# Optimization experiments

Hardware: AMD Instinct MI355X
Metric: run time of the kernel (lower is better)

## Reference

```python
import math
import jax, jax.numpy as jnp
import numpy as np

N_NODES = 50000
N_EDGES = 800000
F_IN = 512
HID = 64
N_CLS = 64
NITER = 10


def setup_inputs() -> dict:
    key = jax.random.key(0)
    k = jax.random.split(key, 6)
    x = jax.random.normal(k[0], (N_NODES, F_IN), jnp.float32)
    edge_index = jax.random.randint(k[1], (2, N_EDGES), 0, N_NODES, jnp.int64)
    W1 = jax.random.normal(k[2], (F_IN, HID), jnp.float32) / np.sqrt(F_IN)
    b1 = jnp.zeros((HID,), jnp.float32)
    W2 = jax.random.normal(k[3], (HID, N_CLS), jnp.float32) / np.sqrt(HID)
    b2 = jnp.zeros((N_CLS,), jnp.float32)
    halt_w = jax.random.normal(k[4], (N_CLS,), jnp.float32) / np.sqrt(N_CLS)
    # reset_parameters: bias = log((1/(niter+1)) / (1 - 1/(niter+1)))
    b = math.log((1.0 / (NITER + 1)) / (1.0 - 1.0 / (NITER + 1)))
    halt_b = jnp.full((1,), b, jnp.float32)
    return {"x": x, "edge_index": edge_index, "W1": W1, "b1": b1,
            "W2": W2, "b2": b2, "halt_w": halt_w, "halt_b": halt_b}


def reference(x, edge_index, W1, b1, W2, b2, halt_w, halt_b):
    N = x.shape[0]
    # MLP (eval mode: dropout is identity)
    h = jnp.maximum(x @ W1 + b1, 0.0)
    local = h @ W2 + b2                      # [N, C] local predictions
    # GCN normalization with self-loops (eval: no edge dropout)
    loops = jnp.arange(N, dtype=edge_index.dtype)
    row = jnp.concatenate([edge_index[0], loops])
    col = jnp.concatenate([edge_index[1], loops])
    deg = jnp.zeros((N,), x.dtype).at[row].add(1.0)
    dis = jnp.where(deg > 0, jax.lax.rsqrt(jnp.maximum(deg, 1.0)), 0.0)
    norm = dis[row] * dis[col]               # [E+N]

    def step(carry, _):
        prop, steps, sum_h, cont, xacc = carry
        old = prop
        msg = norm[:, None] * prop[row]                       # gather + scale
        prop = jax.ops.segment_sum(msg, col, num_segments=N)  # scatter-add
        hh = jax.nn.sigmoid(prop @ halt_w + halt_b[0])        # [N]
        prob = (sum_h + hh < 0.99) & cont
        pf = prob.astype(x.dtype)
        steps = steps + pf
        sum_h = sum_h + pf * hh
        cond = prob & (steps < NITER)
        p = jnp.where(cond, sum_h, 1.0 - sum_h)
        xacc = xacc + (prop * p[:, None] + old * (1.0 - p)[:, None]) * cont.astype(x.dtype)[:, None]
        cont = cont & prob
        return (prop, steps, sum_h, cont, xacc), None

    init = (local, jnp.ones((N,), x.dtype), jnp.zeros((N,), x.dtype),
            jnp.ones((N,), bool), jnp.zeros_like(local))
    (prop, steps, sum_h, cont, xacc), _ = jax.lax.scan(step, init, None, length=NITER)
    out = xacc / steps[:, None]
    return jax.nn.log_softmax(out, axis=1), steps, 1.0 - sum_h
```

## Files before the change

kernel.cpp:

```cpp
#include <hip/hip_runtime.h>
#include <hip/hip_bf16.h>

#define F_IN 512
#define NC 64
#define NITER 10
#define BM 256
#define BK 64

__global__ __launch_bounds__(256) void init_state_kernel(
    float* __restrict__ steps, float* __restrict__ sumh, int* __restrict__ cont,
    int* __restrict__ rowptr, int N, int E) {
  int i = blockIdx.x * blockDim.x + threadIdx.x;
  if (i < N) { steps[i] = 1.0f; sumh[i] = 0.0f; cont[i] = 1; }
  if (i == 0) rowptr[N] = E;
}

__global__ __launch_bounds__(256) void mlp_kernel(
    const float* __restrict__ x, const float* __restrict__ W1,
    const float* __restrict__ b1, const float* __restrict__ W2,
    const float* __restrict__ b2, float* __restrict__ out, int N) {
  __shared__ float xT[BK * BM];
  __shared__ float ws[BK * NC];
  const int tid  = threadIdx.x;
  const int brow = blockIdx.x * BM;
  const int r0 = (tid >> 3) * 8;
  const int c0 = (tid & 7) * 8;

  float acc[8][8];
#pragma unroll
  for (int j = 0; j < 8; ++j) {
    float bv = b1[c0 + j];
#pragma unroll
    for (int i = 0; i < 8; ++i) acc[i][j] = bv;
  }

  for (int kt = 0; kt < F_IN; kt += BK) {
#pragma unroll
    for (int q = 0; q < 16; ++q) {
      int fidx = q * 256 + tid;
      int row = fidx >> 4, kq = fidx & 15;
      int gr = brow + row; if (gr >= N) gr = N - 1;
      float4 v = *reinterpret_cast<const float4*>(&x[(size_t)gr * F_IN + kt + kq * 4]);
      float vv[4] = {v.x, v.y, v.z, v.w};
#pragma unroll
      for (int j = 0; j < 4; ++j) {
        int kk = kq * 4 + j;
        xT[kk * BM + (row ^ (kk & 28))] = vv[j];
      }
    }
#pragma unroll
    for (int q = 0; q < 4; ++q) {
      int fidx = q * 256 + tid;
      int row = fidx >> 4, kq = fidx & 15;
      *reinterpret_cast<float4*>(&ws[row * NC + kq * 4]) =
          *reinterpret_cast<const float4*>(&W1[(size_t)(kt + row) * NC + kq * 4]);
    }
    __syncthreads();
#pragma unroll 4
    for (int k = 0; k < BK; ++k) {
      float4 xa = *reinterpret_cast<const float4*>(&xT[k * BM + (r0 ^ (k & 28))]);
      float4 xb = *reinterpret_cast<const float4*>(&xT[k * BM + ((r0 + 4) ^ (k & 28))]);
      float4 wa = *reinterpret_cast<const float4*>(&ws[k * NC + c0]);
      float4 wb = *reinterpret_cast<const float4*>(&ws[k * NC + c0 + 4]);
      float xr[8] = {xa.x, xa.y, xa.z, xa.w, xb.x, xb.y, xb.z, xb.w};
      float wr[8] = {wa.x, wa.y, wa.z, wa.w, wb.x, wb.y, wb.z, wb.w};
#pragma unroll
      for (int i = 0; i < 8; ++i)
#pragma unroll
        for (int j = 0; j < 8; ++j) acc[i][j] = fmaf(xr[i], wr[j], acc[i][j]);
    }
    __syncthreads();
  }

#pragma unroll
  for (int i = 0; i < 8; ++i)
#pragma unroll
    for (int j = 0; j < 8; ++j) {
      int kk = c0 + j;
      int r  = r0 + i;
      xT[kk * BM + (r ^ (kk & 28))] = fmaxf(acc[i][j], 0.0f);
    }
#pragma unroll
  for (int q = 0; q < 4; ++q) {
    int fidx = q * 256 + tid;
    int row = fidx >> 4, kq = fidx & 15;
    *reinterpret_cast<float4*>(&ws[row * NC + kq * 4]) =
        *reinterpret_cast<const float4*>(&W2[(size_t)row * NC + kq * 4]);
  }
  float acc2[8][8];
#pragma unroll
  for (int j = 0; j < 8; ++j) {
    float bv = b2[c0 + j];
#pragma unroll
    for (int i = 0; i < 8; ++i) acc2[i][j] = bv;
  }
  __syncthreads();
#pragma unroll 4
  for (int k = 0; k < NC; ++k) {
    float4 xa = *reinterpret_cast<const float4*>(&xT[k * BM + (r0 ^ (k & 28))]);
    float4 xb = *reinterpret_cast<const float4*>(&xT[k * BM + ((r0 + 4) ^ (k & 28))]);
    float4 wa = *reinterpret_cast<const float4*>(&ws[k * NC + c0]);
    float4 wb = *reinterpret_cast<const float4*>(&ws[k * NC + c0 + 4]);
    float xr[8] = {xa.x, xa.y, xa.z, xa.w, xb.x, xb.y, xb.z, xb.w};
    float wr[8] = {wa.x, wa.y, wa.z, wa.w, wb.x, wb.y, wb.z, wb.w};
#pragma unroll
    for (int i = 0; i < 8; ++i)
#pragma unroll
      for (int j = 0; j < 8; ++j) acc2[i][j] = fmaf(xr[i], wr[j], acc2[i][j]);
  }
#pragma unroll
  for (int i = 0; i < 8; ++i) {
    int gr = brow + r0 + i;
    if (gr < N) {
      float4 oa = make_float4(acc2[i][0], acc2[i][1], acc2[i][2], acc2[i][3]);
      float4 ob = make_float4(acc2[i][4], acc2[i][5], acc2[i][6], acc2[i][7]);
      *reinterpret_cast<float4*>(&out[(size_t)gr * NC + c0]) = oa;
      *reinterpret_cast<float4*>(&out[(size_t)gr * NC + c0 + 4]) = ob;
    }
  }
}

__global__ __launch_bounds__(256) void hist_kernel(
    const int* __restrict__ ei, int* __restrict__ deg_i,
    int* __restrict__ indeg, int E) {
  int e = blockIdx.x * blockDim.x + threadIdx.x;
  if (e < E) {
    atomicAdd(&deg_i[ei[e]], 1);
    atomicAdd(&indeg[ei[E + e]], 1);
  }
}

__global__ __launch_bounds__(256) void dis_kernel(
    const int* __restrict__ deg_i, float* __restrict__ dis, int N) {
  int i = blockIdx.x * blockDim.x + threadIdx.x;
  if (i < N) dis[i] = 1.0f / sqrtf((float)(deg_i[i] + 1));
}

__global__ __launch_bounds__(256) void scan_sum_kernel(
    const int* __restrict__ indeg, int* __restrict__ bsum, int N) {
  __shared__ int sm[256];
  int tid = threadIdx.x;
  int i = blockIdx.x * 256 + tid;
  sm[tid] = (i < N) ? indeg[i] : 0;
  __syncthreads();
  for (int s = 128; s > 0; s >>= 1) {
    if (tid < s) sm[tid] += sm[tid + s];
    __syncthreads();
  }
  if (tid == 0) bsum[blockIdx.x] = sm[0];
}

__global__ __launch_bounds__(256) void scan_bsum_kernel(int* __restrict__ bsum, int nb) {
  __shared__ int sm[256];
  int tid = threadIdx.x;
  int v = (tid < nb) ? bsum[tid] : 0;
  sm[tid] = v;
  __syncthreads();
  for (int s = 1; s < 256; s <<= 1) {
    int t = (tid >= s) ? sm[tid - s] : 0;
    __syncthreads();
    sm[tid] += t;
    __syncthreads();
  }
  if (tid < nb) bsum[tid] = sm[tid] - v;
}

__global__ __launch_bounds__(256) void scan_final_kernel(
    const int* __restrict__ indeg, const int* __restrict__ bsum,
    int* __restrict__ rowptr, int N) {
  __shared__ int sm[256];
  int tid = threadIdx.x;
  int i = blockIdx.x * 256 + tid;
  int v = (i < N) ? indeg[i] : 0;
  sm[tid] = v;
  __syncthreads();
  for (int s = 1; s < 256; s <<= 1) {
    int t = (tid >= s) ? sm[tid - s] : 0;
    __syncthreads();
    sm[tid] += t;
    __syncthreads();
  }
  if (i < N) rowptr[i] = bsum[blockIdx.x] + sm[tid] - v;
}

__global__ __launch_bounds__(256) void scatter_kernel(
    const int* __restrict__ ei, const int* __restrict__ rowptr,
    int* __restrict__ cursor, const float* __restrict__ dis,
    int2* __restrict__ csr, int E) {
  int e = blockIdx.x * blockDim.x + threadIdx.x;
  if (e < E) {
    int s = ei[e];
    int c = ei[E + e];
    int pos = rowptr[c] + atomicAdd(&cursor[c], 1);
    csr[pos] = make_int2(s, __float_as_int(dis[s] * dis[c]));
  }
}

__global__ __launch_bounds__(256) void prop_step_kernel(
    const float* __restrict__ prop, float* __restrict__ prop_new,
    const int2* __restrict__ csr, const int* __restrict__ rowptr,
    const float* __restrict__ dis, const float* __restrict__ hw,
    const float* __restrict__ hb, float* __restrict__ steps,
    float* __restrict__ sumh, int* __restrict__ cont,
    float* __restrict__ xacc, int N) {
  int wid = (int)((blockIdx.x * blockDim.x + threadIdx.x) >> 6);
  if (wid >= N) return;
  int lane = threadIdx.x & 63;
  size_t rowoff = (size_t)wid * NC + lane;

  float oldv = prop[rowoff];
  float dc = dis[wid];
  int beg = __builtin_amdgcn_readfirstlane(rowptr[wid]);
  int end = __builtin_amdgcn_readfirstlane(rowptr[wid + 1]);

  float a[8];
  a[0] = dc * dc * oldv;
#pragma unroll
  for (int u = 1; u < 8; ++u) a[u] = 0.0f;
  int i = beg;
  for (; i + 8 <= end; i += 8) {
    int2 e[8];
#pragma unroll
    for (int u = 0; u < 8; ++u) e[u] = csr[i + u];
#pragma unroll
    for (int u = 0; u < 8; ++u)
      a[u] = fmaf(__int_as_float(e[u].y), prop[(size_t)e[u].x * NC + lane], a[u]);
  }
  for (; i < end; ++i) {
    int2 e0 = csr[i];
    a[0] = fmaf(__int_as_float(e0.y), prop[(size_t)e0.x * NC + lane], a[0]);
  }
  float acc = ((a[0] + a[1]) + (a[2] + a[3])) + ((a[4] + a[5]) + (a[6] + a[7]));
  prop_new[rowoff] = acc;

  float z = acc * hw[lane];
#pragma unroll
  for (int off = 32; off > 0; off >>= 1) z += __shfl_xor(z, off);
  z += hb[0];
  float hh = 1.0f / (1.0f + expf(-z));

  float st = steps[wid], sh = sumh[wid];
  int ct = cont[wid];
  bool prob = ((sh + hh) < 0.99f) && (ct != 0);
  float pf = prob ? 1.0f : 0.0f;
  st += pf;
  sh += pf * hh;
  bool cond = prob && (st < (float)NITER);
  float pp = cond ? sh : (1.0f - sh);
  float ctf = ct ? 1.0f : 0.0f;
  xacc[rowoff] += (acc * pp + oldv * (1.0f - pp)) * ctf;
  if (lane == 0) { steps[wid] = st; sumh[wid] = sh; cont[wid] = prob ? 1 : 0; }
}

__global__ __launch_bounds__(256) void final_kernel(
    const float* __restrict__ xacc, const float* __restrict__ steps,
    const float* __restrict__ sumh, float* __restrict__ out0,
    float* __restrict__ out1, float* __restrict__ out2, int N) {
  int wid = (int)((blockIdx.x * blockDim.x + threadIdx.x) >> 6);
  if (wid >= N) return;
  int lane = threadIdx.x & 63;
  float st = steps[wid];
  float v = xacc[(size_t)wid * NC + lane] / st;
  float m = v;
#pragma unroll
  for (int off = 32; off > 0; off >>= 1) m = fmaxf(m, __shfl_xor(m, off));
  float e = expf(v - m);
  float s = e;
#pragma unroll
  for (int off = 32; off > 0; off >>= 1) s += __shfl_xor(s, off);
  out0[(size_t)wid * NC + lane] = v - m - logf(s);
  if (lane == 0) { out1[wid] = st; out2[wid] = 1.0f - sumh[wid]; }
}

extern "C" void kernel_launch(void* const* d_in, const int* in_sizes, int n_in,
                              void* d_out, int out_size, void* d_ws, size_t ws_size,
                              hipStream_t stream) {
  const float* x      = (const float*)d_in[0];
  const int*   ei     = (const int*)d_in[1];
  const float* W1     = (const float*)d_in[2];
  const float* b1     = (const float*)d_in[3];
  const float* W2     = (const float*)d_in[4];
  const float* b2     = (const float*)d_in[5];
  const float* halt_w = (const float*)d_in[6];
  const float* halt_b = (const float*)d_in[7];

  const int N = in_sizes[0] / F_IN;
  const int E = in_sizes[1] / 2;

  char* p = (char*)d_ws;
  auto alloc = [&](size_t bytes) {
    void* r = (void*)p;
    p += (bytes + 255) & ~(size_t)255;
    return r;
  };
  float* propA  = (float*)alloc((size_t)N * NC * 4);
  float* propB  = (float*)alloc((size_t)N * NC * 4);
  float* xacc   = (float*)alloc((size_t)N * NC * 4);
  int2*  csr    = (int2*)alloc((size_t)E * 8);
  int*   rowptr = (int*)alloc((size_t)(N + 1) * 4);
  int*   deg_i  = (int*)alloc((size_t)N * 4);
  int*   indeg  = (int*)alloc((size_t)N * 4);
  int*   cursor = (int*)alloc((size_t)N * 4);
  float* dis    = (float*)alloc((size_t)N * 4);
  float* steps  = (float*)alloc((size_t)N * 4);
  float* sumh   = (float*)alloc((size_t)N * 4);
  int*   cont   = (int*)alloc((size_t)N * 4);
  int*   bsum   = (int*)alloc(1024);

  hipMemsetAsync(deg_i,  0, (size_t)N * 4, stream);
  hipMemsetAsync(indeg,  0, (size_t)N * 4, stream);
  hipMemsetAsync(cursor, 0, (size_t)N * 4, stream);
  hipMemsetAsync(xacc,   0, (size_t)N * NC * 4, stream);

  const int nbN = (N + 255) / 256;
  const int nbE = (E + 255) / 256;
  const int nbM = (N + BM - 1) / BM;

  init_state_kernel<<<nbN, 256, 0, stream>>>(steps, sumh, cont, rowptr, N, E);
  mlp_kernel<<<nbM, 256, 0, stream>>>(x, W1, b1, W2, b2, propA, N);
  hist_kernel<<<nbE, 256, 0, stream>>>(ei, deg_i, indeg, E);
  dis_kernel<<<nbN, 256, 0, stream>>>(deg_i, dis, N);
  scan_sum_kernel<<<nbN, 256, 0, stream>>>(indeg, bsum, N);
  scan_bsum_kernel<<<1, 256, 0, stream>>>(bsum, nbN);
  scan_final_kernel<<<nbN, 256, 0, stream>>>(indeg, bsum, rowptr, N);
  scatter_kernel<<<nbE, 256, 0, stream>>>(ei, rowptr, cursor, dis, csr, E);

  float* out0 = (float*)d_out;
  float* out1 = out0 + (size_t)N * NC;
  float* out2 = out1 + N;

  const float* cur = propA;
  float* nxt = propB;
  const int nbW = (N + 3) / 4;
  for (int it = 0; it < NITER; ++it) {
    prop_step_kernel<<<nbW, 256, 0, stream>>>(cur, nxt, csr, rowptr, dis,
                                              halt_w, halt_b, steps, sumh,
                                              cont, xacc, N);
    const float* t = nxt; nxt = (float*)cur; cur = t;
  }
  final_kernel<<<nbW, 256, 0, stream>>>(xacc, steps, sumh, out0, out1, out2, N);
}
```

Measured before the change: 593.1 us.

## Pad CSR rows to multiples of eight and re-tile MLP with row-major swizzled smem

CSR row segments are now padded to multiples of 8 with zeroed entries, so the propagation loop runs only the unrolled 8-wide gather and drops the scalar tail loop. The padded entries point at node 0 with weight 0, which adds a few wasted gathers and an extra memset of the larger CSR buffer. Separately, the MLP kernel moves to 128-row, 128-thread blocks that store x row-major with an XOR swizzle and use float4 reads along k. This removes the per-element transposed shared-memory stores but changes occupancy and the LDS access pattern.

```diff
diff --git a/kernel.cpp b/kernel.cpp
--- a/kernel.cpp
+++ b/kernel.cpp
@@ -4,27 +4,28 @@
 #define F_IN 512
 #define NC 64
 #define NITER 10
-#define BM 256
-#define BK 64
+#define BM 128
 
 __global__ __launch_bounds__(256) void init_state_kernel(
     float* __restrict__ steps, float* __restrict__ sumh, int* __restrict__ cont,
-    int* __restrict__ rowptr, int N, int E) {
+    int N) {
   int i = blockIdx.x * blockDim.x + threadIdx.x;
   if (i < N) { steps[i] = 1.0f; sumh[i] = 0.0f; cont[i] = 1; }
-  if (i == 0) rowptr[N] = E;
-}
-
-__global__ __launch_bounds__(256) void mlp_kernel(
+}
+
+__global__ __launch_bounds__(128) void mlp_kernel(
     const float* __restrict__ x, const float* __restrict__ W1,
     const float* __restrict__ b1, const float* __restrict__ W2,
     const float* __restrict__ b2, float* __restrict__ out, int N) {
-  __shared__ float xT[BK * BM];
-  __shared__ float ws[BK * NC];
+  __shared__ float xs[BM * NC];
+  __shared__ float ws[NC * NC];
   const int tid  = threadIdx.x;
   const int brow = blockIdx.x * BM;
-  const int r0 = (tid >> 3) * 8;
-  const int c0 = (tid & 7) * 8;
+  const int rg = tid >> 3;
+  const int cg = tid & 7;
+  const int r0 = rg * 8;
+  const int c0 = cg * 8;
+  const int keyr = rg & 7;
 
   float acc[8][8];
 #pragma unroll
@@ -34,58 +35,60 @@
     for (int i = 0; i < 8; ++i) acc[i][j] = bv;
   }
 
-  for (int kt = 0; kt < F_IN; kt += BK) {
+  for (int kt = 0; kt < F_IN; kt += 64) {
 #pragma unroll
     for (int q = 0; q < 16; ++q) {
-      int fidx = q * 256 + tid;
-      int row = fidx >> 4, kq = fidx & 15;
+      int c = q * 128 + tid;
+      int row = c >> 4, kc = c & 15;
       int gr = brow + row; if (gr >= N) gr = N - 1;
-      float4 v = *reinterpret_cast<const float4*>(&x[(size_t)gr * F_IN + kt + kq * 4]);
-      float vv[4] = {v.x, v.y, v.z, v.w};
-#pragma unroll
-      for (int j = 0; j < 4; ++j) {
-        int kk = kq * 4 + j;
-        xT[kk * BM + (row ^ (kk & 28))] = vv[j];
+      float4 v = *reinterpret_cast<const float4*>(&x[(size_t)gr * F_IN + kt + kc * 4]);
+      *reinterpret_cast<float4*>(&xs[row * NC + ((kc ^ ((row >> 3) & 7)) << 2)]) = v;
+    }
+#pragma unroll
+    for (int q = 0; q < 8; ++q) {
+      int c = q * 128 + tid;
+      *reinterpret_cast<float4*>(&ws[c * 4]) =
+          *reinterpret_cast<const float4*>(&W1[(size_t)kt * NC + c * 4]);
+    }
+    __syncthreads();
+#pragma unroll 4
+    for (int kc = 0; kc < 16; ++kc) {
+      float xv[8][4];
+#pragma unroll
+      for (int i = 0; i < 8; ++i) {
+        float4 t = *reinterpret_cast<const float4*>(
+            &xs[(r0 + i) * NC + ((kc ^ keyr) << 2)]);
+        xv[i][0] = t.x; xv[i][1] = t.y; xv[i][2] = t.z; xv[i][3] = t.w;
       }
-    }
-#pragma unroll
-    for (int q = 0; q < 4; ++q) {
-      int fidx = q * 256 + tid;
-      int row = fidx >> 4, kq = fidx & 15;
-      *reinterpret_cast<float4*>(&ws[row * NC + kq * 4]) =
-          *reinterpret_cast<const float4*>(&W1[(size_t)(kt + row) * NC + kq * 4]);
-    }
-    __syncthreads();
-#pragma unroll 4
-    for (int k = 0; k < BK; ++k) {
-      float4 xa = *reinterpret_cast<const float4*>(&xT[k * BM + (r0 ^ (k & 28))]);
-      float4 xb = *reinterpret_cast<const float4*>(&xT[k * BM + ((r0 + 4) ^ (k & 28))]);
-      float4 wa = *reinterpret_cast<const float4*>(&ws[k * NC + c0]);
-      float4 wb = *reinterpret_cast<const float4*>(&ws[k * NC + c0 + 4]);
-      float xr[8] = {xa.x, xa.y, xa.z, xa.w, xb.x, xb.y, xb.z, xb.w};
-      float wr[8] = {wa.x, wa.y, wa.z, wa.w, wb.x, wb.y, wb.z, wb.w};
-#pragma unroll
-      for (int i = 0; i < 8; ++i)
-#pragma unroll
-        for (int j = 0; j < 8; ++j) acc[i][j] = fmaf(xr[i], wr[j], acc[i][j]);
-    }
-    __syncthreads();
-  }
-
-#pragma unroll
-  for (int i = 0; i < 8; ++i)
-#pragma unroll
-    for (int j = 0; j < 8; ++j) {
-      int kk = c0 + j;
-      int r  = r0 + i;
-      xT[kk * BM + (r ^ (kk & 28))] = fmaxf(acc[i][j], 0.0f);
-    }
-#pragma unroll
-  for (int q = 0; q < 4; ++q) {
-    int fidx = q * 256 + tid;
-    int row = fidx >> 4, kq = fidx & 15;
-    *reinterpret_cast<float4*>(&ws[row * NC + kq * 4]) =
-        *reinterpret_cast<const float4*>(&W2[(size_t)row * NC + kq * 4]);
+#pragma unroll
+      for (int m = 0; m < 4; ++m) {
+        float4 wa = *reinterpret_cast<const float4*>(&ws[(kc * 4 + m) * NC + c0]);
+        float4 wb = *reinterpret_cast<const float4*>(&ws[(kc * 4 + m) * NC + c0 + 4]);
+        float wr[8] = {wa.x, wa.y, wa.z, wa.w, wb.x, wb.y, wb.z, wb.w};
+#pragma unroll
+        for (int i = 0; i < 8; ++i)
+#pragma unroll
+          for (int j = 0; j < 8; ++j)
+            acc[i][j] = fmaf(xv[i][m], wr[j], acc[i][j]);
+      }
+    }
+    __syncthreads();
+  }
+
+#pragma unroll
+  for (int i = 0; i < 8; ++i) {
+    float4 ha = make_float4(fmaxf(acc[i][0], 0.f), fmaxf(acc[i][1], 0.f),
+                            fmaxf(acc[i][2], 0.f), fmaxf(acc[i][3], 0.f));
+    float4 hb = make_float4(fmaxf(acc[i][4], 0.f), fmaxf(acc[i][5], 0.f),
+                            fmaxf(acc[i][6], 0.f), fmaxf(acc[i][7], 0.f));
+    *reinterpret_cast<float4*>(&xs[(r0 + i) * NC + (((cg * 2 + 0) ^ keyr) << 2)]) = ha;
+    *reinterpret_cast<float4*>(&xs[(r0 + i) * NC + (((cg * 2 + 1) ^ keyr) << 2)]) = hb;
+  }
+#pragma unroll
+  for (int q = 0; q < 8; ++q) {
+    int c = q * 128 + tid;
+    *reinterpret_cast<float4*>(&ws[c * 4]) =
+        *reinterpret_cast<const float4*>(&W2[c * 4]);
   }
   float acc2[8][8];
 #pragma unroll
@@ -96,17 +99,25 @@
   }
   __syncthreads();
 #pragma unroll 4
-  for (int k = 0; k < NC; ++k) {
-    float4 xa = *reinterpret_cast<const float4*>(&xT[k * BM + (r0 ^ (k & 28))]);
-    float4 xb = *reinterpret_cast<const float4*>(&xT[k * BM + ((r0 + 4) ^ (k & 28))]);
-    float4 wa = *reinterpret_cast<const float4*>(&ws[k * NC + c0]);
-    float4 wb = *reinterpret_cast<const float4*>(&ws[k * NC + c0 + 4]);
-    float xr[8] = {xa.x, xa.y, xa.z, xa.w, xb.x, xb.y, xb.z, xb.w};
-    float wr[8] = {wa.x, wa.y, wa.z, wa.w, wb.x, wb.y, wb.z, wb.w};
-#pragma unroll
-    for (int i = 0; i < 8; ++i)
-#pragma unroll
-      for (int j = 0; j < 8; ++j) acc2[i][j] = fmaf(xr[i], wr[j], acc2[i][j]);
+  for (int kc = 0; kc < 16; ++kc) {
+    float xv[8][4];
+#pragma unroll
+    for (int i = 0; i < 8; ++i) {
+      float4 t = *reinterpret_cast<const float4*>(
+          &xs[(r0 + i) * NC + ((kc ^ keyr) << 2)]);
+      xv[i][0] = t.x; xv[i][1] = t.y; xv[i][2] = t.z; xv[i][3] = t.w;
+    }
+#pragma unroll
+    for (int m = 0; m < 4; ++m) {
+      float4 wa = *reinterpret_cast<const float4*>(&ws[(kc * 4 + m) * NC + c0]);
+      float4 wb = *reinterpret_cast<const float4*>(&ws[(kc * 4 + m) * NC + c0 + 4]);
+      float wr[8] = {wa.x, wa.y, wa.z, wa.w, wb.x, wb.y, wb.z, wb.w};
+#pragma unroll
+      for (int i = 0; i < 8; ++i)
+#pragma unroll
+        for (int j = 0; j < 8; ++j)
+          acc2[i][j] = fmaf(xv[i][m], wr[j], acc2[i][j]);
+    }
   }
 #pragma unroll
   for (int i = 0; i < 8; ++i) {
@@ -136,12 +147,14 @@
   if (i < N) dis[i] = 1.0f / sqrtf((float)(deg_i[i] + 1));
 }
 
+__device__ __forceinline__ int pad8(int v) { return (v + 7) & ~7; }
+
 __global__ __launch_bounds__(256) void scan_sum_kernel(
     const int* __restrict__ indeg, int* __restrict__ bsum, int N) {
   __shared__ int sm[256];
   int tid = threadIdx.x;
   int i = blockIdx.x * 256 + tid;
-  sm[tid] = (i < N) ? indeg[i] : 0;
+  sm[tid] = (i < N) ? pad8(indeg[i]) : 0;
   __syncthreads();
   for (int s = 128; s > 0; s >>= 1) {
     if (tid < s) sm[tid] += sm[tid + s];
@@ -171,7 +184,7 @@
   __shared__ int sm[256];
   int tid = threadIdx.x;
   int i = blockIdx.x * 256 + tid;
-  int v = (i < N) ? indeg[i] : 0;
+  int v = (i < N) ? pad8(indeg[i]) : 0;
   sm[tid] = v;
   __syncthreads();
   for (int s = 1; s < 256; s <<= 1) {
@@ -180,7 +193,10 @@
     sm[tid] += t;
     __syncthreads();
   }
-  if (i < N) rowptr[i] = bsum[blockIdx.x] + sm[tid] - v;
+  if (i < N) {
+    rowptr[i] = bsum[blockIdx.x] + sm[tid] - v;
+    if (i == N - 1) rowptr[N] = bsum[blockIdx.x] + sm[tid];
+  }
 }
 
 __global__ __launch_bounds__(256) void scatter_kernel(
@@ -217,18 +233,13 @@
   a[0] = dc * dc * oldv;
 #pragma unroll
   for (int u = 1; u < 8; ++u) a[u] = 0.0f;
-  int i = beg;
-  for (; i + 8 <= end; i += 8) {
+  for (int i = beg; i < end; i += 8) {
     int2 e[8];
 #pragma unroll
     for (int u = 0; u < 8; ++u) e[u] = csr[i + u];
 #pragma unroll
     for (int u = 0; u < 8; ++u)
       a[u] = fmaf(__int_as_float(e[u].y), prop[(size_t)e[u].x * NC + lane], a[u]);
-  }
-  for (; i < end; ++i) {
-    int2 e0 = csr[i];
-    a[0] = fmaf(__int_as_float(e0.y), prop[(size_t)e0.x * NC + lane], a[0]);
   }
   float acc = ((a[0] + a[1]) + (a[2] + a[3])) + ((a[4] + a[5]) + (a[6] + a[7]));
   prop_new[rowoff] = acc;
@@ -286,6 +297,7 @@
 
   const int N = in_sizes[0] / F_IN;
   const int E = in_sizes[1] / 2;
+  const int EP = E + 8 * N;
 
   char* p = (char*)d_ws;
   auto alloc = [&](size_t bytes) {
@@ -296,7 +308,7 @@
   float* propA  = (float*)alloc((size_t)N * NC * 4);
   float* propB  = (float*)alloc((size_t)N * NC * 4);
   float* xacc   = (float*)alloc((size_t)N * NC * 4);
-  int2*  csr    = (int2*)alloc((size_t)E * 8);
+  int2*  csr    = (int2*)alloc((size_t)EP * 8);
   int*   rowptr = (int*)alloc((size_t)(N + 1) * 4);
   int*   deg_i  = (int*)alloc((size_t)N * 4);
   int*   indeg  = (int*)alloc((size_t)N * 4);
@@ -311,13 +323,14 @@
   hipMemsetAsync(indeg,  0, (size_t)N * 4, stream);
   hipMemsetAsync(cursor, 0, (size_t)N * 4, stream);
   hipMemsetAsync(xacc,   0, (size_t)N * NC * 4, stream);
+  hipMemsetAsync(csr,    0, (size_t)EP * 8, stream);
 
   const int nbN = (N + 255) / 256;
   const int nbE = (E + 255) / 256;
   const int nbM = (N + BM - 1) / BM;
 
-  init_state_kernel<<<nbN, 256, 0, stream>>>(steps, sumh, cont, rowptr, N, E);
-  mlp_kernel<<<nbM, 256, 0, stream>>>(x, W1, b1, W2, b2, propA, N);
+  init_state_kernel<<<nbN, 256, 0, stream>>>(steps, sumh, cont, N);
+  mlp_kernel<<<nbM, 128, 0, stream>>>(x, W1, b1, W2, b2, propA, N);
   hist_kernel<<<nbE, 256, 0, stream>>>(ei, deg_i, indeg, E);
   dis_kernel<<<nbN, 256, 0, stream>>>(deg_i, dis, N);
   scan_sum_kernel<<<nbN, 256, 0, stream>>>(indeg, bsum, N);
```

New measurement: 580.4 us. -2.1%, faster.
